# Kernel tuning notes

Hardware: AMD Instinct MI355X
Metric: run time of the kernel (lower is better)

## Reference

```python
import jax, jax.numpy as jnp
import numpy as np

IN_DIM, OUT_DIM = 4096, 11008
NUM_SUBDIM, KS = 1376, 256
DS = OUT_DIM // NUM_SUBDIM  # 8
BATCH = 32


def setup_inputs() -> dict:
    key = jax.random.key(0)
    k1, k2, k3, k4 = jax.random.split(key, 4)
    x = jax.random.normal(k1, (BATCH, IN_DIM), dtype=jnp.float32)
    vectors = jax.random.normal(k2, (NUM_SUBDIM, KS, DS), dtype=jnp.float32)
    bias = jax.random.normal(k3, (OUT_DIM,), dtype=jnp.float32)
    indexes = jax.random.randint(k4, (IN_DIM, NUM_SUBDIM), 0, KS, dtype=jnp.int64)
    return {"x": x, "vectors": vectors, "bias": bias, "indexes": indexes}


def reference(x, vectors, bias, indexes):
    in_dim, num_subdim = indexes.shape
    ds = vectors.shape[-1]
    # PQ dequant: gather codewords per (row, subspace) -> [in_dim, num_subdim, Ds]
    # vectors[d, indexes[i, d]] via broadcast of arange(num_subdim) against indexes.
    dims = jnp.arange(num_subdim)
    weight = vectors[dims, indexes].reshape(in_dim, num_subdim * ds)  # [in_dim, out_dim]
    return x @ weight + bias
```

## Files before the change

### kernel.cpp

```cpp
#include <hip/hip_runtime.h>

#define IN_DIM  4096
#define OUT_DIM 11008
#define NSUB    1376
#define KSQ     256
#define DSUB    8
#define BATCH   32

#define DTILE   16
#define NTILE   128
#define KC      128
#define KSPLIT  16
#define KPB     (IN_DIM / KSPLIT)
#define NCHUNK  (KPB / KC)
#define NBLK    (OUT_DIM / NTILE)

typedef unsigned short ushort_t;
typedef unsigned int   uint_t;
typedef __attribute__((ext_vector_type(8))) short bf16x8;
typedef __attribute__((ext_vector_type(4))) float f32x4;

#define SW_STRIDE 136
#define SX_STRIDE 136
#define SI_STRIDE 132

#define VEC_N   (NSUB * KSQ * DSUB)
#define XBF_OFF 5636096
#define PREP_V  (VEC_N / 2)
#define PREP_X  (BATCH * IN_DIM / 2)
#define PREP_O  (BATCH * OUT_DIM)
#define PREP_N  (PREP_V + PREP_X + PREP_O)

__device__ __forceinline__ ushort_t f2bf(float f) {
    union { float f; uint_t u; } a; a.f = f;
    uint_t u = a.u;
    u += 0x7fffu + ((u >> 16) & 1u);
    return (ushort_t)(u >> 16);
}

__global__ __launch_bounds__(256) void pq_prep(
    const float* __restrict__ x, const float* __restrict__ vecs,
    const float* __restrict__ bias,
    uint_t* __restrict__ vbf, uint_t* __restrict__ xbf, float* __restrict__ out)
{
    int tid = blockIdx.x * 256 + threadIdx.x;
    if (tid < PREP_V) {
        float2 v = ((const float2*)vecs)[tid];
        vbf[tid] = (uint_t)f2bf(v.x) | ((uint_t)f2bf(v.y) << 16);
    } else if (tid < PREP_V + PREP_X) {
        int i = tid - PREP_V;
        float2 v = ((const float2*)x)[i];
        xbf[i] = (uint_t)f2bf(v.x) | ((uint_t)f2bf(v.y) << 16);
    } else {
        int i = tid - (PREP_V + PREP_X);
        out[i] = bias[i % OUT_DIM];
    }
}

__global__ __launch_bounds__(256) void pq_main(
    const ushort_t* __restrict__ xbf, const uint4* __restrict__ vbf,
    const int* __restrict__ idx, float* __restrict__ out)
{
    __shared__ ushort_t sW[NTILE * SW_STRIDE];
    __shared__ ushort_t sX[BATCH * SX_STRIDE];
    __shared__ int      sI[DTILE * SI_STRIDE];

    const int t    = threadIdx.x;
    const int nblk = blockIdx.x;
    const int kblk = blockIdx.y;
    const int d0   = nblk * DTILE;
    const int kbase = kblk * KPB;

    const int wave = t >> 6;
    const int lane = t & 63;
    const int l15  = lane & 15;
    const int l4   = lane >> 4;

    const int gd = t >> 4;
    const int go = t & 15;

    f32x4 acc[2][2];
    #pragma unroll
    for (int i = 0; i < 2; ++i)
        #pragma unroll
        for (int j = 0; j < 2; ++j)
            acc[i][j] = (f32x4)0.0f;

    int   ireg[8];
    uint4 xreg[2];

    {
        const int i0 = kbase;
        #pragma unroll
        for (int p = 0; p < 8; ++p) {
            int f = p * 256 + t, ii = f >> 4, dd = f & 15;
            ireg[p] = idx[(size_t)(i0 + ii) * NSUB + (d0 + dd)];
        }
        #pragma unroll
        for (int p = 0; p < 2; ++p) {
            int f = p * 256 + t, b = f >> 4, q = f & 15;
            xreg[p] = ((const uint4*)xbf)[b * (IN_DIM / 8) + i0 / 8 + q];
        }
    }

    for (int c = 0; c < NCHUNK; ++c) {
        __syncthreads();

        #pragma unroll
        for (int p = 0; p < 8; ++p) {
            int f = p * 256 + t, ii = f >> 4, dd = f & 15;
            sI[dd * SI_STRIDE + ii] = ireg[p];
        }
        #pragma unroll
        for (int p = 0; p < 2; ++p) {
            int f = p * 256 + t, b = f >> 4, q = f & 15;
            *(uint4*)&sX[b * SX_STRIDE + q * 8] = xreg[p];
        }
        __syncthreads();

        int kk[8];
        #pragma unroll
        for (int s = 0; s < 8; ++s)
            kk[s] = sI[gd * SI_STRIDE + go * 8 + s];

        uint4 q[8];
        #pragma unroll
        for (int s = 0; s < 8; ++s)
            q[s] = vbf[(d0 + gd) * KSQ + kk[s]];

        if (c + 1 < NCHUNK) {
            const int i0n = kbase + (c + 1) * KC;
            #pragma unroll
            for (int p = 0; p < 8; ++p) {
                int f = p * 256 + t, ii = f >> 4, dd = f & 15;
                ireg[p] = idx[(size_t)(i0n + ii) * NSUB + (d0 + dd)];
            }
            #pragma unroll
            for (int p = 0; p < 2; ++p) {
                int f = p * 256 + t, b = f >> 4, qq = f & 15;
                xreg[p] = ((const uint4*)xbf)[b * (IN_DIM / 8) + i0n / 8 + qq];
            }
        }

        #pragma unroll
        for (int j = 0; j < 8; ++j) {
            const uint_t sel = (j & 1) ? 0x07060302u : 0x05040100u;
            uint_t c0 = (j >> 1) == 0 ? q[0].x : (j >> 1) == 1 ? q[0].y : (j >> 1) == 2 ? q[0].z : q[0].w;
            uint_t c1 = (j >> 1) == 0 ? q[1].x : (j >> 1) == 1 ? q[1].y : (j >> 1) == 2 ? q[1].z : q[1].w;
            uint_t c2 = (j >> 1) == 0 ? q[2].x : (j >> 1) == 1 ? q[2].y : (j >> 1) == 2 ? q[2].z : q[2].w;
            uint_t c3 = (j >> 1) == 0 ? q[3].x : (j >> 1) == 1 ? q[3].y : (j >> 1) == 2 ? q[3].z : q[3].w;
            uint_t c4 = (j >> 1) == 0 ? q[4].x : (j >> 1) == 1 ? q[4].y : (j >> 1) == 2 ? q[4].z : q[4].w;
            uint_t c5 = (j >> 1) == 0 ? q[5].x : (j >> 1) == 1 ? q[5].y : (j >> 1) == 2 ? q[5].z : q[5].w;
            uint_t c6 = (j >> 1) == 0 ? q[6].x : (j >> 1) == 1 ? q[6].y : (j >> 1) == 2 ? q[6].z : q[6].w;
            uint_t c7 = (j >> 1) == 0 ? q[7].x : (j >> 1) == 1 ? q[7].y : (j >> 1) == 2 ? q[7].z : q[7].w;
            uint4 wv;
            wv.x = __builtin_amdgcn_perm(c1, c0, sel);
            wv.y = __builtin_amdgcn_perm(c3, c2, sel);
            wv.z = __builtin_amdgcn_perm(c5, c4, sel);
            wv.w = __builtin_amdgcn_perm(c7, c6, sel);
            *(uint4*)&sW[(gd * 8 + j) * SW_STRIDE + go * 8] = wv;
        }
        __syncthreads();

        #pragma unroll
        for (int kq = 0; kq < KC / 32; ++kq) {
            bf16x8 A[2], B[2];
            #pragma unroll
            for (int mt = 0; mt < 2; ++mt)
                A[mt] = *(const bf16x8*)
                    &sX[(mt * 16 + l15) * SX_STRIDE + kq * 32 + l4 * 8];
            #pragma unroll
            for (int nt = 0; nt < 2; ++nt)
                B[nt] = *(const bf16x8*)
                    &sW[(wave * 32 + nt * 16 + l15) * SW_STRIDE + kq * 32 + l4 * 8];
            #pragma unroll
            for (int mt = 0; mt < 2; ++mt)
                #pragma unroll
                for (int nt = 0; nt < 2; ++nt)
                    acc[mt][nt] = __builtin_amdgcn_mfma_f32_16x16x32_bf16(
                        A[mt], B[nt], acc[mt][nt], 0, 0, 0);
        }
    }

    #pragma unroll
    for (int mt = 0; mt < 2; ++mt)
        #pragma unroll
        for (int nt = 0; nt < 2; ++nt)
            #pragma unroll
            for (int r = 0; r < 4; ++r) {
                int row = mt * 16 + l4 * 4 + r;
                int col = nblk * NTILE + wave * 32 + nt * 16 + l15;
                atomicAdd(&out[(size_t)row * OUT_DIM + col], acc[mt][nt][r]);
            }
}

extern "C" void kernel_launch(void* const* d_in, const int* in_sizes, int n_in,
                              void* d_out, int out_size, void* d_ws, size_t ws_size,
                              hipStream_t stream) {
    const float* x    = (const float*)d_in[0];
    const float* vecs = (const float*)d_in[1];
    const float* bias = (const float*)d_in[2];
    const int*   idx  = (const int*)d_in[3];
    float* out = (float*)d_out;

    uint_t* vbf = (uint_t*)d_ws;
    uint_t* xbf = (uint_t*)((char*)d_ws + XBF_OFF);

    pq_prep<<<PREP_N / 256, 256, 0, stream>>>(x, vecs, bias, vbf, xbf, out);
    dim3 grid(NBLK, KSPLIT);
    pq_main<<<grid, 256, 0, stream>>>((const ushort_t*)xbf, (const uint4*)vbf,
                                      idx, out);
}
```

Before: 115.4 us.

## Stage per-block codebooks in shared memory and shrink tile with fewer K splits

Each block now preloads the full 256-entry bf16 codebooks for its 8 subspaces into LDS and looks codewords up there, instead of issuing random global gathers into the codebook. The N tile is halved to 64 and KSPLIT is cut from 16 to 4, so each block runs more K chunks and amortises the codebook load, with fewer atomic partial sums to the output. Index loads become one int4 per thread. In exchange, LDS use per block grows by 32 KB, which may limit occupancy, and each wave now issues only two MFMAs per k-step.

```diff
diff --git a/kernel.cpp b/kernel.cpp
--- a/kernel.cpp
+++ b/kernel.cpp
@@ -7,10 +7,10 @@
 #define DSUB    8
 #define BATCH   32
 
-#define DTILE   16
-#define NTILE   128
+#define DTILE   8
+#define NTILE   64
 #define KC      128
-#define KSPLIT  16
+#define KSPLIT  4
 #define KPB     (IN_DIM / KSPLIT)
 #define NCHUNK  (KPB / KC)
 #define NBLK    (OUT_DIM / NTILE)
@@ -61,6 +61,7 @@
     const ushort_t* __restrict__ xbf, const uint4* __restrict__ vbf,
     const int* __restrict__ idx, float* __restrict__ out)
 {
+    __shared__ uint4    sCB[DTILE * KSQ];
     __shared__ ushort_t sW[NTILE * SW_STRIDE];
     __shared__ ushort_t sX[BATCH * SX_STRIDE];
     __shared__ int      sI[DTILE * SI_STRIDE];
@@ -76,122 +77,95 @@
     const int l15  = lane & 15;
     const int l4   = lane >> 4;
 
-    const int gd = t >> 4;
-    const int go = t & 15;
+    const int gd = t >> 5;
+    const int go = t & 31;
 
-    f32x4 acc[2][2];
-    #pragma unroll
-    for (int i = 0; i < 2; ++i)
-        #pragma unroll
-        for (int j = 0; j < 2; ++j)
-            acc[i][j] = (f32x4)0.0f;
+    const int ii0 = t >> 1;
+    const int g0  = t & 1;
 
-    int   ireg[8];
-    uint4 xreg[2];
+    f32x4 acc[2];
+    acc[0] = (f32x4)0.0f;
+    acc[1] = (f32x4)0.0f;
 
     {
-        const int i0 = kbase;
+        const uint4* vb = vbf + (size_t)d0 * KSQ;
         #pragma unroll
-        for (int p = 0; p < 8; ++p) {
-            int f = p * 256 + t, ii = f >> 4, dd = f & 15;
-            ireg[p] = idx[(size_t)(i0 + ii) * NSUB + (d0 + dd)];
-        }
-        #pragma unroll
-        for (int p = 0; p < 2; ++p) {
-            int f = p * 256 + t, b = f >> 4, q = f & 15;
-            xreg[p] = ((const uint4*)xbf)[b * (IN_DIM / 8) + i0 / 8 + q];
-        }
+        for (int p = 0; p < 8; ++p)
+            sCB[p * 256 + t] = vb[p * 256 + t];
+    }
+
+    int4  ireg;
+    uint4 xreg[2];
+    ireg = *(const int4*)&idx[(size_t)(kbase + ii0) * NSUB + d0 + g0 * 4];
+    #pragma unroll
+    for (int p = 0; p < 2; ++p) {
+        int f = p * 256 + t, b = f >> 4, qx = f & 15;
+        xreg[p] = ((const uint4*)xbf)[b * (IN_DIM / 8) + kbase / 8 + qx];
     }
 
     for (int c = 0; c < NCHUNK; ++c) {
         __syncthreads();
 
-        #pragma unroll
-        for (int p = 0; p < 8; ++p) {
-            int f = p * 256 + t, ii = f >> 4, dd = f & 15;
-            sI[dd * SI_STRIDE + ii] = ireg[p];
-        }
+        sI[(g0 * 4 + 0) * SI_STRIDE + ii0] = ireg.x;
+        sI[(g0 * 4 + 1) * SI_STRIDE + ii0] = ireg.y;
+        sI[(g0 * 4 + 2) * SI_STRIDE + ii0] = ireg.z;
+        sI[(g0 * 4 + 3) * SI_STRIDE + ii0] = ireg.w;
         #pragma unroll
         for (int p = 0; p < 2; ++p) {
-            int f = p * 256 + t, b = f >> 4, q = f & 15;
-            *(uint4*)&sX[b * SX_STRIDE + q * 8] = xreg[p];
+            int f = p * 256 + t, b = f >> 4, qx = f & 15;
+            *(uint4*)&sX[b * SX_STRIDE + qx * 8] = xreg[p];
+        }
+
+        if (c + 1 < NCHUNK) {
+            const int i0n = kbase + (c + 1) * KC;
+            ireg = *(const int4*)&idx[(size_t)(i0n + ii0) * NSUB + d0 + g0 * 4];
+            #pragma unroll
+            for (int p = 0; p < 2; ++p) {
+                int f = p * 256 + t, b = f >> 4, qx = f & 15;
+                xreg[p] = ((const uint4*)xbf)[b * (IN_DIM / 8) + i0n / 8 + qx];
+            }
         }
         __syncthreads();
 
-        int kk[8];
-        #pragma unroll
-        for (int s = 0; s < 8; ++s)
-            kk[s] = sI[gd * SI_STRIDE + go * 8 + s];
-
-        uint4 q[8];
-        #pragma unroll
-        for (int s = 0; s < 8; ++s)
-            q[s] = vbf[(d0 + gd) * KSQ + kk[s]];
-
-        if (c + 1 < NCHUNK) {
-            const int i0n = kbase + (c + 1) * KC;
-            #pragma unroll
-            for (int p = 0; p < 8; ++p) {
-                int f = p * 256 + t, ii = f >> 4, dd = f & 15;
-                ireg[p] = idx[(size_t)(i0n + ii) * NSUB + (d0 + dd)];
-            }
-            #pragma unroll
-            for (int p = 0; p < 2; ++p) {
-                int f = p * 256 + t, b = f >> 4, qq = f & 15;
-                xreg[p] = ((const uint4*)xbf)[b * (IN_DIM / 8) + i0n / 8 + qq];
-            }
-        }
+        int4 kk = *(const int4*)&sI[gd * SI_STRIDE + go * 4];
+        uint4 q0 = sCB[gd * KSQ + kk.x];
+        uint4 q1 = sCB[gd * KSQ + kk.y];
+        uint4 q2 = sCB[gd * KSQ + kk.z];
+        uint4 q3 = sCB[gd * KSQ + kk.w];
 
         #pragma unroll
         for (int j = 0; j < 8; ++j) {
             const uint_t sel = (j & 1) ? 0x07060302u : 0x05040100u;
-            uint_t c0 = (j >> 1) == 0 ? q[0].x : (j >> 1) == 1 ? q[0].y : (j >> 1) == 2 ? q[0].z : q[0].w;
-            uint_t c1 = (j >> 1) == 0 ? q[1].x : (j >> 1) == 1 ? q[1].y : (j >> 1) == 2 ? q[1].z : q[1].w;
-            uint_t c2 = (j >> 1) == 0 ? q[2].x : (j >> 1) == 1 ? q[2].y : (j >> 1) == 2 ? q[2].z : q[2].w;
-            uint_t c3 = (j >> 1) == 0 ? q[3].x : (j >> 1) == 1 ? q[3].y : (j >> 1) == 2 ? q[3].z : q[3].w;
-            uint_t c4 = (j >> 1) == 0 ? q[4].x : (j >> 1) == 1 ? q[4].y : (j >> 1) == 2 ? q[4].z : q[4].w;
-            uint_t c5 = (j >> 1) == 0 ? q[5].x : (j >> 1) == 1 ? q[5].y : (j >> 1) == 2 ? q[5].z : q[5].w;
-            uint_t c6 = (j >> 1) == 0 ? q[6].x : (j >> 1) == 1 ? q[6].y : (j >> 1) == 2 ? q[6].z : q[6].w;
-            uint_t c7 = (j >> 1) == 0 ? q[7].x : (j >> 1) == 1 ? q[7].y : (j >> 1) == 2 ? q[7].z : q[7].w;
-            uint4 wv;
+            const int cc = j >> 1;
+            uint_t c0 = cc == 0 ? q0.x : cc == 1 ? q0.y : cc == 2 ? q0.z : q0.w;
+            uint_t c1 = cc == 0 ? q1.x : cc == 1 ? q1.y : cc == 2 ? q1.z : q1.w;
+            uint_t c2 = cc == 0 ? q2.x : cc == 1 ? q2.y : cc == 2 ? q2.z : q2.w;
+            uint_t c3 = cc == 0 ? q3.x : cc == 1 ? q3.y : cc == 2 ? q3.z : q3.w;
+            uint2 wv;
             wv.x = __builtin_amdgcn_perm(c1, c0, sel);
             wv.y = __builtin_amdgcn_perm(c3, c2, sel);
-            wv.z = __builtin_amdgcn_perm(c5, c4, sel);
-            wv.w = __builtin_amdgcn_perm(c7, c6, sel);
-            *(uint4*)&sW[(gd * 8 + j) * SW_STRIDE + go * 8] = wv;
+            *(uint2*)&sW[(gd * 8 + j) * SW_STRIDE + go * 4] = wv;
         }
         __syncthreads();
 
         #pragma unroll
         for (int kq = 0; kq < KC / 32; ++kq) {
-            bf16x8 A[2], B[2];
-            #pragma unroll
-            for (int mt = 0; mt < 2; ++mt)
-                A[mt] = *(const bf16x8*)
-                    &sX[(mt * 16 + l15) * SX_STRIDE + kq * 32 + l4 * 8];
-            #pragma unroll
-            for (int nt = 0; nt < 2; ++nt)
-                B[nt] = *(const bf16x8*)
-                    &sW[(wave * 32 + nt * 16 + l15) * SW_STRIDE + kq * 32 + l4 * 8];
-            #pragma unroll
-            for (int mt = 0; mt < 2; ++mt)
-                #pragma unroll
-                for (int nt = 0; nt < 2; ++nt)
-                    acc[mt][nt] = __builtin_amdgcn_mfma_f32_16x16x32_bf16(
-                        A[mt], B[nt], acc[mt][nt], 0, 0, 0);
+            bf16x8 A0 = *(const bf16x8*)&sX[(l15) * SX_STRIDE + kq * 32 + l4 * 8];
+            bf16x8 A1 = *(const bf16x8*)&sX[(16 + l15) * SX_STRIDE + kq * 32 + l4 * 8];
+            bf16x8 B  = *(const bf16x8*)&sW[(wave * 16 + l15) * SW_STRIDE + kq * 32 + l4 * 8];
+            acc[0] = __builtin_amdgcn_mfma_f32_16x16x32_bf16(A0, B, acc[0], 0, 0, 0);
+            acc[1] = __builtin_amdgcn_mfma_f32_16x16x32_bf16(A1, B, acc[1], 0, 0, 0);
         }
     }
 
     #pragma unroll
     for (int mt = 0; mt < 2; ++mt)
         #pragma unroll
-        for (int nt = 0; nt < 2; ++nt)
-            #pragma unroll
-            for (int r = 0; r < 4; ++r) {
-                int row = mt * 16 + l4 * 4 + r;
-                int col = nblk * NTILE + wave * 32 + nt * 16 + l15;
-                atomicAdd(&out[(size_t)row * OUT_DIM + col], acc[mt][nt][r]);
-            }
+        for (int r = 0; r < 4; ++r) {
+            int row = mt * 16 + l4 * 4 + r;
+            int col = nblk * NTILE + wave * 16 + l15;
+            atomicAdd(&out[(size_t)row * OUT_DIM + col], acc[mt][r]);
+        }
 }
 
 extern "C" void kernel_launch(void* const* d_in, const int* in_sizes, int n_in,
```

Result: slower. 121.0 us (+4.8%).
